# Optimization experiments

Hardware: AMD Instinct MI355X
Metric: run time of the kernel (lower is better)

## Reference

```python
import jax, jax.numpy as jnp
import numpy as np

H = 64   # hidden_dim
E = 5    # num_edge_features
F = 6    # num_node_features
B, W, N = 8, 12, 200
LN_EPS = 1e-5


def _lstm_layer(x, Wih, Whh, bih, bhh):
    # x: [BN, W, Fin] -> full output sequence [BN, W, H] (PyTorch gate order i,f,g,o)
    BN = x.shape[0]
    h0 = jnp.zeros((BN, Whh.shape[1]), x.dtype)
    def step(carry, xt):
        h, c = carry
        g = xt @ Wih.T + h @ Whh.T + (bih + bhh)
        i, f, gg, o = jnp.split(g, 4, axis=-1)
        c = jax.nn.sigmoid(f) * c + jax.nn.sigmoid(i) * jnp.tanh(gg)
        h = jax.nn.sigmoid(o) * jnp.tanh(c)
        return (h, c), h
    _, ys = jax.lax.scan(step, (h0, h0), jnp.swapaxes(x, 0, 1))
    return jnp.swapaxes(ys, 0, 1)


def _layernorm(x, g, b):
    mu = jnp.mean(x, axis=-1, keepdims=True)
    var = jnp.mean(jnp.square(x - mu), axis=-1, keepdims=True)
    return (x - mu) * jax.lax.rsqrt(var + LN_EPS) * g + b


def setup_inputs() -> dict:
    key = jax.random.key(0)
    ks = jax.random.split(key, 32)
    s = 0.05
    d = {
        'node_features': jax.random.normal(ks[0], (B, W, N, F), jnp.float32),
        'edge_features': jax.random.normal(ks[1], (B, W, N, N, E), jnp.float32),
        'adjacency': jax.random.uniform(ks[2], (B, N, N), jnp.float32),
        # LSTM layer 0 (input F) and layer 1 (input H)
        'Wih0': jax.random.normal(ks[3], (4 * H, F), jnp.float32) * s,
        'Whh0': jax.random.normal(ks[4], (4 * H, H), jnp.float32) * s,
        'bih0': jax.random.normal(ks[5], (4 * H,), jnp.float32) * s,
        'bhh0': jax.random.normal(ks[6], (4 * H,), jnp.float32) * s,
        'Wih1': jax.random.normal(ks[7], (4 * H, H), jnp.float32) * s,
        'Whh1': jax.random.normal(ks[8], (4 * H, H), jnp.float32) * s,
        'bih1': jax.random.normal(ks[9], (4 * H,), jnp.float32) * s,
        'bhh1': jax.random.normal(ks[10], (4 * H,), jnp.float32) * s,
        # 2 GCN layers: linear, edge projection, layernorm
        'gcn_W': jax.random.normal(ks[11], (2, H, H), jnp.float32) * s,
        'gcn_b': jax.random.normal(ks[12], (2, H), jnp.float32) * s,
        'ep_W': jax.random.normal(ks[13], (2, H, E), jnp.float32) * s,
        'ep_b': jax.random.normal(ks[14], (2, H), jnp.float32) * s,
        'ln_g': jnp.ones((2, H), jnp.float32),
        'ln_b': jnp.zeros((2, H), jnp.float32),
        # edge MLP: (2H+E) -> H -> H//2 -> 1
        'mlp_W1': jax.random.normal(ks[15], (H, 2 * H + E), jnp.float32) * s,
        'mlp_b1': jax.random.normal(ks[16], (H,), jnp.float32) * s,
        'mlp_W2': jax.random.normal(ks[17], (H // 2, H), jnp.float32) * s,
        'mlp_b2': jax.random.normal(ks[18], (H // 2,), jnp.float32) * s,
        'mlp_W3': jax.random.normal(ks[19], (1, H // 2), jnp.float32) * s,
        'mlp_b3': jax.random.normal(ks[20], (1,), jnp.float32) * s,
    }
    return d


def reference(node_features, edge_features, adjacency,
              Wih0, Whh0, bih0, bhh0, Wih1, Whh1, bih1, bhh1,
              gcn_W, gcn_b, ep_W, ep_b, ln_g, ln_b,
              mlp_W1, mlp_b1, mlp_W2, mlp_b2, mlp_W3, mlp_b3):
    Bn, Wn, Nn, _ = node_features.shape
    # [B,W,N,F] -> [B*N, W, F]
    x = jnp.transpose(node_features, (0, 2, 1, 3)).reshape(Bn * Nn, Wn, -1)
    y0 = _lstm_layer(x, Wih0, Whh0, bih0, bhh0)      # dropout between layers: eval mode (identity)
    y1 = _lstm_layer(y0, Wih1, Whh1, bih1, bhh1)
    h = y1[:, -1, :].reshape(Bn, Nn, H)

    edge_last = edge_features[:, -1]                 # [B,N,N,E]
    for i in range(2):
        edge_h = edge_last @ ep_W[i].T + ep_b[i]     # [B,N,N,H]
        messages = jnp.einsum('bij,bijn->bin', adjacency, edge_h)
        updated = h @ gcn_W[i].T + gcn_b[i] + messages
        h = jax.nn.relu(_layernorm(updated, ln_g[i], ln_b[i]))
        # dropout: eval mode (identity)

    h_i = jnp.broadcast_to(h[:, :, None, :], (Bn, Nn, Nn, H))
    h_j = jnp.broadcast_to(h[:, None, :, :], (Bn, Nn, Nn, H))
    edge_input = jnp.concatenate([h_i, h_j, edge_last], axis=-1)  # [B,N,N,2H+E]
    z = jax.nn.relu(edge_input @ mlp_W1.T + mlp_b1)
    z = jax.nn.relu(z @ mlp_W2.T + mlp_b2)
    logits = (z @ mlp_W3.T + mlp_b3)[..., 0]
    return jax.nn.sigmoid(logits)
```

## Files before the change

### kernel.cpp

```cpp
#include <hip/hip_runtime.h>
#include <math.h>


#define Hd   64
#define Ed   5
#define Fd   6
#define Bd   8
#define Wd   12
#define Nd   200
#define NSEQ (Bd*Nd)
#define NG   (4*Hd)
#define NEDGE (Bd*Nd*Nd)
#define LNEPS 1e-5f

__device__ __forceinline__ float sigm(float x) { return 1.0f / (1.0f + __expf(-x)); }
__device__ __forceinline__ float tanh_fast(float x) {
  float ax = fabsf(x);
  float t  = __expf(-2.0f * ax);
  float r  = (1.0f - t) / (1.0f + t);
  return copysignf(r, x);
}

__global__ __launch_bounds__(256) void k_prep(
    const float* __restrict__ Wih1, const float* __restrict__ gcn_W,
    const float* __restrict__ ep_W, const float* __restrict__ W1,
    float* __restrict__ Wt1, float* __restrict__ gcnWT,
    float* __restrict__ epWT, float* __restrict__ W1aT,
    float* __restrict__ W1bT)
{
  int idx = blockIdx.x * 256 + threadIdx.x;
  if (idx < 16384) {
    int k = idx >> 8, j = idx & 255;
    Wt1[idx] = Wih1[j * Hd + k];
  } else if (idx < 24576) {
    int r0 = idx - 16384;
    int round = r0 >> 12, rem = r0 & 4095;
    int k = rem >> 6, u = rem & 63;
    gcnWT[r0] = gcn_W[round * 4096 + u * 64 + k];
  } else if (idx < 25216) {
    int r0 = idx - 24576;
    int round = r0 / 320, rem = r0 % 320;
    int e = rem >> 6, u = rem & 63;
    epWT[r0] = ep_W[round * 320 + u * Ed + e];
  } else if (idx < 29312) {
    int r0 = idx - 25216;
    int k = r0 >> 6, n = r0 & 63;
    W1aT[r0] = W1[n * 133 + k];
  } else if (idx < 33408) {
    int r0 = idx - 29312;
    int k = r0 >> 6, n = r0 & 63;
    W1bT[r0] = W1[n * 133 + 64 + k];
  }
}

__global__ __launch_bounds__(256, 3) void k_lstm0(
    const float* __restrict__ nf,
    const float* __restrict__ Wih0, const float* __restrict__ Whh0,
    const float* __restrict__ bih0, const float* __restrict__ bhh0,
    float* __restrict__ y0)
{
  __shared__ float x_sh[Wd * Fd];
  __shared__ float h_sh[Hd];
  __shared__ float gate_sh[2][NG];

  const int tid = threadIdx.x;
  const int seq = blockIdx.x;
  const int b = seq / Nd, n = seq % Nd;
  const int u = tid & 63;

  if (tid < Wd * Fd) {
    int t = tid / Fd, f = tid % Fd;
    x_sh[tid] = nf[((b * Wd + t) * Nd + n) * Fd + f];
  }
  h_sh[u] = 0.f;

  const int j = tid;
  float4 wh[16];
  const float4* wrow = (const float4*)(Whh0 + j * Hd);
  #pragma unroll
  for (int q = 0; q < 16; ++q) wh[q] = wrow[q];
  float wx[Fd];
  #pragma unroll
  for (int f = 0; f < Fd; ++f) wx[f] = Wih0[j * Fd + f];
  const float bias = bih0[j] + bhh0[j];
  const int jt = j >> 6;

  float c = 0.f;
  float yreg[Wd];
  __syncthreads();

  for (int t = 0; t < Wd; ++t) {
    const float* xp = x_sh + t * Fd;
    float a0 = bias, a1 = 0.f, a2 = 0.f, a3 = 0.f;
    #pragma unroll
    for (int f = 0; f < Fd; ++f) a1 += xp[f] * wx[f];
    const float4* h4 = (const float4*)h_sh;
    #pragma unroll
    for (int q = 0; q < 16; ++q) {
      float4 hv = h4[q];
      float d = hv.x * wh[q].x + hv.y * wh[q].y + hv.z * wh[q].z + hv.w * wh[q].w;
      if ((q & 3) == 0) a0 += d; else if ((q & 3) == 1) a1 += d;
      else if ((q & 3) == 2) a2 += d; else a3 += d;
    }
    float acc = (a0 + a1) + (a2 + a3);
    gate_sh[t & 1][j] = (jt == 2) ? tanh_fast(acc) : sigm(acc);
    __syncthreads();
    const float* gb = gate_sh[t & 1];
    float iv = gb[u];
    float fv = gb[64 + u];
    float gv = gb[128 + u];
    float ov = gb[192 + u];
    c = fv * c + iv * gv;
    float h = ov * tanh_fast(c);
    h_sh[u] = h;
    yreg[t] = h;
  }
  if (tid < Hd) {
    #pragma unroll
    for (int t = 0; t < Wd; ++t)
      y0[seq * (Wd * Hd) + t * Hd + u] = yreg[t];
  }
}

__global__ __launch_bounds__(256) void k_xproj1(
    const float* __restrict__ y0,
    const float* __restrict__ Wt1,
    const float* __restrict__ bih1, const float* __restrict__ bhh1,
    float* __restrict__ G1)
{
  __shared__ float ysh[64 * 65];
  __shared__ float osh[2 * 64 * 65];

  const int tid  = threadIdx.x;
  const int row0 = blockIdx.x * 64;
  for (int idx = tid; idx < 64 * 64; idx += 256) {
    int r = idx >> 6, k = idx & 63;
    ysh[r * 65 + k] = y0[(row0 + r) * Hd + k];
  }
  __syncthreads();

  const int w = __builtin_amdgcn_readfirstlane(tid >> 6);
  const int r = tid & 63;
  float acc[64];
  #pragma unroll
  for (int c = 0; c < 64; ++c) acc[c] = 0.f;

  const float* wbase = Wt1 + (w << 6);
  #pragma unroll 2
  for (int k = 0; k < 64; ++k) {
    float yv = ysh[r * 65 + k];
    const float* wk = wbase + k * NG;
    #pragma unroll
    for (int c = 0; c < 64; ++c) acc[c] = fmaf(yv, wk[c], acc[c]);
  }
  #pragma unroll
  for (int c = 0; c < 64; ++c) acc[c] += bih1[(w << 6) + c] + bhh1[(w << 6) + c];

  #pragma unroll
  for (int p = 0; p < 2; ++p) {
    __syncthreads();
    if ((w >> 1) == p) {
      float* orow = osh + ((w & 1) * 64 + r) * 65;
      #pragma unroll
      for (int c = 0; c < 64; ++c) orow[c] = acc[c];
    }
    __syncthreads();
    for (int idx = tid; idx < 2 * 64 * 64; idx += 256) {
      int c  = idx & 127;
      int rr = idx >> 7;
      G1[(row0 + rr) * NG + p * 128 + c] =
          osh[((c >> 6) * 64 + rr) * 65 + (c & 63)];
    }
  }
}

__global__ __launch_bounds__(256, 3) void k_lstm1(
    const float* __restrict__ G1,
    const float* __restrict__ Whh1,
    float* __restrict__ hout)
{
  __shared__ float h_sh[Hd];
  __shared__ float gate_sh[2][NG];

  const int tid = threadIdx.x;
  const int seq = blockIdx.x;
  const int u = tid & 63;
  h_sh[u] = 0.f;

  const int j = tid;
  float4 wh[16];
  const float4* wrow = (const float4*)(Whh1 + j * Hd);
  #pragma unroll
  for (int q = 0; q < 16; ++q) wh[q] = wrow[q];
  const int jt = j >> 6;
  float c = 0.f;
  float hlast = 0.f;

  float g_cur = G1[(seq * Wd + 0) * NG + j];
  __syncthreads();

  for (int t = 0; t < Wd; ++t) {
    float g_next = (t + 1 < Wd) ? G1[(seq * Wd + t + 1) * NG + j] : 0.f;
    float a0 = g_cur;
    float a1 = 0.f, a2 = 0.f, a3 = 0.f;
    const float4* h4 = (const float4*)h_sh;
    #pragma unroll
    for (int q = 0; q < 16; ++q) {
      float4 hv = h4[q];
      float d = hv.x * wh[q].x + hv.y * wh[q].y + hv.z * wh[q].z + hv.w * wh[q].w;
      if ((q & 3) == 0) a0 += d; else if ((q & 3) == 1) a1 += d;
      else if ((q & 3) == 2) a2 += d; else a3 += d;
    }
    float acc = (a0 + a1) + (a2 + a3);
    gate_sh[t & 1][j] = (jt == 2) ? tanh_fast(acc) : sigm(acc);
    __syncthreads();
    const float* gb = gate_sh[t & 1];
    float iv = gb[u];
    float fv = gb[64 + u];
    float gv = gb[128 + u];
    float ov = gb[192 + u];
    c = fv * c + iv * gv;
    float h = ov * tanh_fast(c);
    h_sh[u] = h;
    hlast = h;
    g_cur = g_next;
  }
  if (tid < Hd) hout[seq * Hd + u] = hlast;
}

__global__ __launch_bounds__(256) void k_node(
    const float* __restrict__ ef,    const float* __restrict__ adj,
    const float* __restrict__ h0,
    const float* __restrict__ gcnWT, const float* __restrict__ gcn_b,
    const float* __restrict__ epWT,  const float* __restrict__ ep_b,
    const float* __restrict__ ln_g,  const float* __restrict__ ln_b,
    const float* __restrict__ W1aT,  const float* __restrict__ W1bT,
    const float* __restrict__ b1,
    float* __restrict__ uu, float* __restrict__ vt)
{
  __shared__ float ef_sh[Nd * Ed];
  __shared__ float adj_sh[Nd];
  __shared__ float red[4][6];
  __shared__ float w6[6];
  __shared__ float hcur[Hd];

  const int row = blockIdx.x;
  const int b = row / Nd, i = row % Nd;
  const int tid = threadIdx.x;

  const float* efrow = ef + (size_t)(((b * Wd + (Wd - 1)) * Nd + i)) * (Nd * Ed);
  for (int idx = tid; idx < Nd * Ed; idx += 256) ef_sh[idx] = efrow[idx];
  const float* adjrow = adj + (b * Nd + i) * Nd;
  if (tid < Nd) adj_sh[tid] = adjrow[tid];
  if (tid < Hd) hcur[tid] = h0[row * Hd + tid];
  __syncthreads();

  float p[6] = {0.f, 0.f, 0.f, 0.f, 0.f, 0.f};
  if (tid < Nd) {
    float a = adj_sh[tid];
    p[5] = a;
    #pragma unroll
    for (int k = 0; k < Ed; ++k) p[k] = a * ef_sh[tid * Ed + k];
  }
  #pragma unroll
  for (int k = 0; k < 6; ++k) {
    float v = p[k];
    for (int off = 32; off > 0; off >>= 1) v += __shfl_down(v, off);
    p[k] = v;
  }
  if ((tid & 63) == 0) {
    #pragma unroll
    for (int k = 0; k < 6; ++k) red[tid >> 6][k] = p[k];
  }
  __syncthreads();
  if (tid < 6)
    w6[tid] = red[0][tid] + red[1][tid] + red[2][tid] + red[3][tid];
  __syncthreads();

  const int u = tid & 63;
  #pragma unroll
  for (int round = 0; round < 2; ++round) {
    float hnew = 0.f;
    if (tid < 64) {
      const float* gwT = gcnWT + round * 4096;
      const float* ewT = epWT  + round * 320;
      float acc = gcn_b[round * Hd + u] + w6[5] * ep_b[round * Hd + u];
      #pragma unroll
      for (int e = 0; e < Ed; ++e) acc += w6[e] * ewT[e * 64 + u];
      #pragma unroll 8
      for (int k = 0; k < Hd; ++k) acc += hcur[k] * gwT[k * 64 + u];

      float mu = acc;
      #pragma unroll
      for (int off = 1; off < 64; off <<= 1) mu += __shfl_xor(mu, off);
      mu *= (1.f / 64.f);
      float d = acc - mu;
      float var = d * d;
      #pragma unroll
      for (int off = 1; off < 64; off <<= 1) var += __shfl_xor(var, off);
      var *= (1.f / 64.f);
      float v = d * rsqrtf(var + LNEPS) * ln_g[round * Hd + u] + ln_b[round * Hd + u];
      hnew = fmaxf(v, 0.f);
    }
    __syncthreads();
    if (tid < 64) hcur[tid] = hnew;
    __syncthreads();
  }

  if (tid < 64) {
    float acc = b1[tid];
    #pragma unroll 8
    for (int k = 0; k < Hd; ++k) acc += hcur[k] * W1aT[k * 64 + tid];
    uu[row * Hd + tid] = acc;
  } else if (tid < 128) {
    const int n = tid - 64;
    float acc = 0.f;
    #pragma unroll 8
    for (int k = 0; k < Hd; ++k) acc += hcur[k] * W1bT[k * 64 + n];
    vt[n * NSEQ + row] = acc;
  }
}

__global__ __launch_bounds__(256) void k_mlp(
    const float* __restrict__ ef,
    const float* __restrict__ u, const float* __restrict__ vt,
    const float* __restrict__ W1,
    const float* __restrict__ W2, const float* __restrict__ b2,
    const float* __restrict__ W3, const float* __restrict__ b3,
    float* __restrict__ out)
{
  const int idx = blockIdx.x * 256 + threadIdx.x;
  const int b   = idx / (Nd * Nd);
  const int rem = idx - b * Nd * Nd;
  const int i   = rem / Nd;
  const int jj  = rem - i * Nd;

  const float* e = ef + (((b * Wd + (Wd - 1)) * Nd + i) * Nd + jj) * Ed;
  float e5[Ed];
  #pragma unroll
  for (int q = 0; q < Ed; ++q) e5[q] = e[q];

  const float* ur = u + (b * Nd + i) * Hd;
  const int vcol = b * Nd + jj;

  float z1[64];
  #pragma unroll
  for (int k = 0; k < 64; ++k) {
    float acc = ur[k] + vt[k * NSEQ + vcol];
    const float* w1c = W1 + k * 133 + 128;
    #pragma unroll
    for (int q = 0; q < Ed; ++q) acc += e5[q] * w1c[q];
    z1[k] = fmaxf(acc, 0.f);
  }

  float logit = b3[0];
  #pragma unroll 4
  for (int o = 0; o < 32; ++o) {
    float a0 = b2[o], a1 = 0.f, a2 = 0.f, a3 = 0.f;
    const float* w2 = W2 + o * 64;
    #pragma unroll
    for (int k = 0; k < 64; k += 4) {
      a0 += w2[k]     * z1[k];
      a1 += w2[k + 1] * z1[k + 1];
      a2 += w2[k + 2] * z1[k + 2];
      a3 += w2[k + 3] * z1[k + 3];
    }
    float z2 = fmaxf((a0 + a1) + (a2 + a3), 0.f);
    logit += W3[o] * z2;
  }
  out[idx] = 1.f / (1.f + __expf(-logit));
}

extern "C" void kernel_launch(void* const* d_in, const int* in_sizes, int n_in,
                              void* d_out, int out_size, void* d_ws, size_t ws_size,
                              hipStream_t stream) {
  (void)in_sizes; (void)n_in; (void)out_size; (void)ws_size;
  const float* nf   = (const float*)d_in[0];
  const float* ef   = (const float*)d_in[1];
  const float* adj  = (const float*)d_in[2];
  const float* Wih0 = (const float*)d_in[3];
  const float* Whh0 = (const float*)d_in[4];
  const float* bih0 = (const float*)d_in[5];
  const float* bhh0 = (const float*)d_in[6];
  const float* Wih1 = (const float*)d_in[7];
  const float* Whh1 = (const float*)d_in[8];
  const float* bih1 = (const float*)d_in[9];
  const float* bhh1 = (const float*)d_in[10];
  const float* gcnW = (const float*)d_in[11];
  const float* gcnB = (const float*)d_in[12];
  const float* epW  = (const float*)d_in[13];
  const float* epB  = (const float*)d_in[14];
  const float* lnG  = (const float*)d_in[15];
  const float* lnB  = (const float*)d_in[16];
  const float* W1   = (const float*)d_in[17];
  const float* b1   = (const float*)d_in[18];
  const float* W2   = (const float*)d_in[19];
  const float* b2   = (const float*)d_in[20];
  const float* W3   = (const float*)d_in[21];
  const float* b3   = (const float*)d_in[22];
  float* out = (float*)d_out;

  float* ws   = (float*)d_ws;
  float* y0   = ws;
  float* G1   = y0   + 1228800;
  float* Wt1  = G1   + 4915200;
  float* h0   = Wt1  + 16384;
  float* uu   = h0   + 102400;
  float* vt   = uu   + 102400;
  float* gWT  = vt   + 102400;
  float* eWT  = gWT  + 8192;
  float* W1aT = eWT  + 640;
  float* W1bT = W1aT + 4096;

  k_prep  <<<131,  256, 0, stream>>>(Wih1, gcnW, epW, W1,
                                     Wt1, gWT, eWT, W1aT, W1bT);
  k_lstm0 <<<NSEQ, 256, 0, stream>>>(nf, Wih0, Whh0, bih0, bhh0, y0);
  k_xproj1<<<300,  256, 0, stream>>>(y0, Wt1, bih1, bhh1, G1);
  k_lstm1 <<<NSEQ, 256, 0, stream>>>(G1, Whh1, h0);
  k_node  <<<1600, 256, 0, stream>>>(ef, adj, h0, gWT, gcnB, eWT, epB,
                                     lnG, lnB, W1aT, W1bT, b1, uu, vt);
  k_mlp   <<<1250, 256, 0, stream>>>(ef, uu, vt, W1, W2, b2, W3, b3, out);
}
```

Measured before the change: 267.8 us.

## Fuse both LSTM layers into one wavefront-pipelined kernel with 8 sequences per block

Replaces the separate layer-0 LSTM, layer-1 input projection and layer-1 LSTM kernels with a single kernel. Threads 0-255 run layer 0 and threads 256-511 run layer 1 one step behind, with layer 1 computing its input projection on the fly from layer 0's hidden state in shared memory. Each block handles 8 sequences so weights held in registers are reused across them. This removes the y0 and G1 global round-trips and two launches, at the cost of more register pressure from the second weight set and serial per-sequence loops inside each timestep.

```diff
diff --git a/kernel.cpp b/kernel.cpp
--- a/kernel.cpp
+++ b/kernel.cpp
@@ -10,7 +10,7 @@
 #define Nd   200
 #define NSEQ (Bd*Nd)
 #define NG   (4*Hd)
-#define NEDGE (Bd*Nd*Nd)
+#define SEQPB 8
 #define LNEPS 1e-5f
 
 __device__ __forceinline__ float sigm(float x) { return 1.0f / (1.0f + __expf(-x)); }
@@ -22,210 +22,176 @@
 }
 
 __global__ __launch_bounds__(256) void k_prep(
-    const float* __restrict__ Wih1, const float* __restrict__ gcn_W,
-    const float* __restrict__ ep_W, const float* __restrict__ W1,
-    float* __restrict__ Wt1, float* __restrict__ gcnWT,
-    float* __restrict__ epWT, float* __restrict__ W1aT,
-    float* __restrict__ W1bT)
+    const float* __restrict__ gcn_W, const float* __restrict__ ep_W,
+    const float* __restrict__ W1,
+    float* __restrict__ gcnWT, float* __restrict__ epWT,
+    float* __restrict__ W1aT, float* __restrict__ W1bT)
 {
   int idx = blockIdx.x * 256 + threadIdx.x;
-  if (idx < 16384) {
-    int k = idx >> 8, j = idx & 255;
-    Wt1[idx] = Wih1[j * Hd + k];
-  } else if (idx < 24576) {
-    int r0 = idx - 16384;
-    int round = r0 >> 12, rem = r0 & 4095;
+  if (idx < 8192) {
+    int round = idx >> 12, rem = idx & 4095;
     int k = rem >> 6, u = rem & 63;
-    gcnWT[r0] = gcn_W[round * 4096 + u * 64 + k];
-  } else if (idx < 25216) {
-    int r0 = idx - 24576;
+    gcnWT[idx] = gcn_W[round * 4096 + u * 64 + k];
+  } else if (idx < 8832) {
+    int r0 = idx - 8192;
     int round = r0 / 320, rem = r0 % 320;
     int e = rem >> 6, u = rem & 63;
     epWT[r0] = ep_W[round * 320 + u * Ed + e];
-  } else if (idx < 29312) {
-    int r0 = idx - 25216;
+  } else if (idx < 12928) {
+    int r0 = idx - 8832;
     int k = r0 >> 6, n = r0 & 63;
     W1aT[r0] = W1[n * 133 + k];
-  } else if (idx < 33408) {
-    int r0 = idx - 29312;
+  } else if (idx < 17024) {
+    int r0 = idx - 12928;
     int k = r0 >> 6, n = r0 & 63;
     W1bT[r0] = W1[n * 133 + 64 + k];
   }
 }
 
-__global__ __launch_bounds__(256, 3) void k_lstm0(
+__global__ __launch_bounds__(512, 2) void k_lstm_fused(
     const float* __restrict__ nf,
     const float* __restrict__ Wih0, const float* __restrict__ Whh0,
     const float* __restrict__ bih0, const float* __restrict__ bhh0,
-    float* __restrict__ y0)
+    const float* __restrict__ Wih1, const float* __restrict__ Whh1,
+    const float* __restrict__ bih1, const float* __restrict__ bhh1,
+    float* __restrict__ hout)
 {
-  __shared__ float x_sh[Wd * Fd];
-  __shared__ float h_sh[Hd];
-  __shared__ float gate_sh[2][NG];
-
-  const int tid = threadIdx.x;
-  const int seq = blockIdx.x;
-  const int b = seq / Nd, n = seq % Nd;
-  const int u = tid & 63;
-
-  if (tid < Wd * Fd) {
-    int t = tid / Fd, f = tid % Fd;
-    x_sh[tid] = nf[((b * Wd + t) * Nd + n) * Fd + f];
-  }
-  h_sh[u] = 0.f;
-
-  const int j = tid;
+  __shared__ float x_sh[SEQPB][Wd * Fd];
+  __shared__ float h0_sh[SEQPB][Hd];
+  __shared__ float h1_sh[SEQPB][Hd];
+  __shared__ float g0_sh[SEQPB][NG];
+  __shared__ float g1_sh[SEQPB][NG];
+
+  const int tid  = threadIdx.x;
+  const int seq0 = blockIdx.x * SEQPB;
+  const int b    = seq0 / Nd;
+  const int n0   = seq0 % Nd;
+
+  for (int idx = tid; idx < SEQPB * Wd * Fd; idx += 512) {
+    int s = idx / (Wd * Fd), r = idx - s * (Wd * Fd);
+    int t = r / Fd, f = r - t * Fd;
+    x_sh[s][r] = nf[((b * Wd + t) * Nd + (n0 + s)) * Fd + f];
+  }
+  ((float*)h0_sh)[tid >= 512 ? 0 : tid] = 0.f;
+  ((float*)h1_sh)[tid >= 512 ? 0 : tid] = 0.f;
+
+  const bool isL0 = (tid < 256);
+  const int j  = tid & 255;
+  const int jt = j >> 6;
+  const int u  = tid & 63;
+  const int w  = (tid >> 6) & 3;
+
   float4 wh[16];
-  const float4* wrow = (const float4*)(Whh0 + j * Hd);
-  #pragma unroll
-  for (int q = 0; q < 16; ++q) wh[q] = wrow[q];
-  float wx[Fd];
-  #pragma unroll
-  for (int f = 0; f < Fd; ++f) wx[f] = Wih0[j * Fd + f];
-  const float bias = bih0[j] + bhh0[j];
-  const int jt = j >> 6;
-
-  float c = 0.f;
-  float yreg[Wd];
+  float4 wi1[16];
+  float  wx[Fd];
+  float  bias;
+  if (isL0) {
+    const float4* wr = (const float4*)(Whh0 + j * Hd);
+    #pragma unroll
+    for (int q = 0; q < 16; ++q) wh[q] = wr[q];
+    #pragma unroll
+    for (int f = 0; f < Fd; ++f) wx[f] = Wih0[j * Fd + f];
+    bias = bih0[j] + bhh0[j];
+  } else {
+    const float4* wr = (const float4*)(Whh1 + j * Hd);
+    #pragma unroll
+    for (int q = 0; q < 16; ++q) wh[q] = wr[q];
+    const float4* xr = (const float4*)(Wih1 + j * Hd);
+    #pragma unroll
+    for (int q = 0; q < 16; ++q) wi1[q] = xr[q];
+    bias = bih1[j] + bhh1[j];
+  }
+
+  float cA = 0.f, cB = 0.f;
+  float hA = 0.f, hB = 0.f;
   __syncthreads();
 
-  for (int t = 0; t < Wd; ++t) {
-    const float* xp = x_sh + t * Fd;
-    float a0 = bias, a1 = 0.f, a2 = 0.f, a3 = 0.f;
-    #pragma unroll
-    for (int f = 0; f < Fd; ++f) a1 += xp[f] * wx[f];
-    const float4* h4 = (const float4*)h_sh;
-    #pragma unroll
-    for (int q = 0; q < 16; ++q) {
-      float4 hv = h4[q];
-      float d = hv.x * wh[q].x + hv.y * wh[q].y + hv.z * wh[q].z + hv.w * wh[q].w;
-      if ((q & 3) == 0) a0 += d; else if ((q & 3) == 1) a1 += d;
-      else if ((q & 3) == 2) a2 += d; else a3 += d;
-    }
-    float acc = (a0 + a1) + (a2 + a3);
-    gate_sh[t & 1][j] = (jt == 2) ? tanh_fast(acc) : sigm(acc);
-    __syncthreads();
-    const float* gb = gate_sh[t & 1];
-    float iv = gb[u];
-    float fv = gb[64 + u];
-    float gv = gb[128 + u];
-    float ov = gb[192 + u];
-    c = fv * c + iv * gv;
-    float h = ov * tanh_fast(c);
-    h_sh[u] = h;
-    yreg[t] = h;
-  }
-  if (tid < Hd) {
-    #pragma unroll
-    for (int t = 0; t < Wd; ++t)
-      y0[seq * (Wd * Hd) + t * Hd + u] = yreg[t];
-  }
-}
-
-__global__ __launch_bounds__(256) void k_xproj1(
-    const float* __restrict__ y0,
-    const float* __restrict__ Wt1,
-    const float* __restrict__ bih1, const float* __restrict__ bhh1,
-    float* __restrict__ G1)
-{
-  __shared__ float ysh[64 * 65];
-  __shared__ float osh[2 * 64 * 65];
-
-  const int tid  = threadIdx.x;
-  const int row0 = blockIdx.x * 64;
-  for (int idx = tid; idx < 64 * 64; idx += 256) {
-    int r = idx >> 6, k = idx & 63;
-    ysh[r * 65 + k] = y0[(row0 + r) * Hd + k];
-  }
-  __syncthreads();
-
-  const int w = __builtin_amdgcn_readfirstlane(tid >> 6);
-  const int r = tid & 63;
-  float acc[64];
-  #pragma unroll
-  for (int c = 0; c < 64; ++c) acc[c] = 0.f;
-
-  const float* wbase = Wt1 + (w << 6);
-  #pragma unroll 2
-  for (int k = 0; k < 64; ++k) {
-    float yv = ysh[r * 65 + k];
-    const float* wk = wbase + k * NG;
-    #pragma unroll
-    for (int c = 0; c < 64; ++c) acc[c] = fmaf(yv, wk[c], acc[c]);
-  }
-  #pragma unroll
-  for (int c = 0; c < 64; ++c) acc[c] += bih1[(w << 6) + c] + bhh1[(w << 6) + c];
-
-  #pragma unroll
-  for (int p = 0; p < 2; ++p) {
-    __syncthreads();
-    if ((w >> 1) == p) {
-      float* orow = osh + ((w & 1) * 64 + r) * 65;
-      #pragma unroll
-      for (int c = 0; c < 64; ++c) orow[c] = acc[c];
+  for (int t = 0; t <= Wd; ++t) {
+    if (isL0) {
+      if (t < Wd) {
+        #pragma unroll 2
+        for (int s = 0; s < SEQPB; ++s) {
+          const float* xp = &x_sh[s][t * Fd];
+          float a0 = bias, a1 = 0.f, a2 = 0.f, a3 = 0.f;
+          #pragma unroll
+          for (int f = 0; f < Fd; ++f) a1 += xp[f] * wx[f];
+          const float4* h4 = (const float4*)h0_sh[s];
+          #pragma unroll
+          for (int q = 0; q < 16; ++q) {
+            float4 hv = h4[q];
+            float d = hv.x * wh[q].x + hv.y * wh[q].y + hv.z * wh[q].z + hv.w * wh[q].w;
+            if ((q & 3) == 0) a0 += d; else if ((q & 3) == 1) a1 += d;
+            else if ((q & 3) == 2) a2 += d; else a3 += d;
+          }
+          float acc = (a0 + a1) + (a2 + a3);
+          g0_sh[s][j] = (jt == 2) ? tanh_fast(acc) : sigm(acc);
+        }
+      }
+    } else {
+      if (t >= 1) {
+        #pragma unroll 2
+        for (int s = 0; s < SEQPB; ++s) {
+          const float4* y4 = (const float4*)h0_sh[s];
+          float xacc = 0.f;
+          #pragma unroll
+          for (int q = 0; q < 16; ++q) {
+            float4 yv = y4[q];
+            xacc = fmaf(yv.x, wi1[q].x, xacc);
+            xacc = fmaf(yv.y, wi1[q].y, xacc);
+            xacc = fmaf(yv.z, wi1[q].z, xacc);
+            xacc = fmaf(yv.w, wi1[q].w, xacc);
+          }
+          xacc += bias;
+          float a0 = xacc, a1 = 0.f, a2 = 0.f, a3 = 0.f;
+          const float4* h4 = (const float4*)h1_sh[s];
+          #pragma unroll
+          for (int q = 0; q < 16; ++q) {
+            float4 hv = h4[q];
+            float d = hv.x * wh[q].x + hv.y * wh[q].y + hv.z * wh[q].z + hv.w * wh[q].w;
+            if ((q & 3) == 0) a0 += d; else if ((q & 3) == 1) a1 += d;
+            else if ((q & 3) == 2) a2 += d; else a3 += d;
+          }
+          float acc = (a0 + a1) + (a2 + a3);
+          g1_sh[s][j] = (jt == 2) ? tanh_fast(acc) : sigm(acc);
+        }
+      }
     }
     __syncthreads();
-    for (int idx = tid; idx < 2 * 64 * 64; idx += 256) {
-      int c  = idx & 127;
-      int rr = idx >> 7;
-      G1[(row0 + rr) * NG + p * 128 + c] =
-          osh[((c >> 6) * 64 + rr) * 65 + (c & 63)];
+
+    if (isL0) {
+      if (t < Wd) {
+        const float* gb = g0_sh[w];
+        float iv = gb[u], fv = gb[64 + u], gv = gb[128 + u], ov = gb[192 + u];
+        cA = fv * cA + iv * gv;
+        hA = ov * tanh_fast(cA);
+        h0_sh[w][u] = hA;
+        const float* gb2 = g0_sh[w + 4];
+        float iv2 = gb2[u], fv2 = gb2[64 + u], gv2 = gb2[128 + u], ov2 = gb2[192 + u];
+        cB = fv2 * cB + iv2 * gv2;
+        hB = ov2 * tanh_fast(cB);
+        h0_sh[w + 4][u] = hB;
+      }
+    } else {
+      if (t >= 1) {
+        const float* gb = g1_sh[w];
+        float iv = gb[u], fv = gb[64 + u], gv = gb[128 + u], ov = gb[192 + u];
+        cA = fv * cA + iv * gv;
+        hA = ov * tanh_fast(cA);
+        h1_sh[w][u] = hA;
+        const float* gb2 = g1_sh[w + 4];
+        float iv2 = gb2[u], fv2 = gb2[64 + u], gv2 = gb2[128 + u], ov2 = gb2[192 + u];
+        cB = fv2 * cB + iv2 * gv2;
+        hB = ov2 * tanh_fast(cB);
+        h1_sh[w + 4][u] = hB;
+      }
     }
-  }
-}
-
-__global__ __launch_bounds__(256, 3) void k_lstm1(
-    const float* __restrict__ G1,
-    const float* __restrict__ Whh1,
-    float* __restrict__ hout)
-{
-  __shared__ float h_sh[Hd];
-  __shared__ float gate_sh[2][NG];
-
-  const int tid = threadIdx.x;
-  const int seq = blockIdx.x;
-  const int u = tid & 63;
-  h_sh[u] = 0.f;
-
-  const int j = tid;
-  float4 wh[16];
-  const float4* wrow = (const float4*)(Whh1 + j * Hd);
-  #pragma unroll
-  for (int q = 0; q < 16; ++q) wh[q] = wrow[q];
-  const int jt = j >> 6;
-  float c = 0.f;
-  float hlast = 0.f;
-
-  float g_cur = G1[(seq * Wd + 0) * NG + j];
-  __syncthreads();
-
-  for (int t = 0; t < Wd; ++t) {
-    float g_next = (t + 1 < Wd) ? G1[(seq * Wd + t + 1) * NG + j] : 0.f;
-    float a0 = g_cur;
-    float a1 = 0.f, a2 = 0.f, a3 = 0.f;
-    const float4* h4 = (const float4*)h_sh;
-    #pragma unroll
-    for (int q = 0; q < 16; ++q) {
-      float4 hv = h4[q];
-      float d = hv.x * wh[q].x + hv.y * wh[q].y + hv.z * wh[q].z + hv.w * wh[q].w;
-      if ((q & 3) == 0) a0 += d; else if ((q & 3) == 1) a1 += d;
-      else if ((q & 3) == 2) a2 += d; else a3 += d;
-    }
-    float acc = (a0 + a1) + (a2 + a3);
-    gate_sh[t & 1][j] = (jt == 2) ? tanh_fast(acc) : sigm(acc);
     __syncthreads();
-    const float* gb = gate_sh[t & 1];
-    float iv = gb[u];
-    float fv = gb[64 + u];
-    float gv = gb[128 + u];
-    float ov = gb[192 + u];
-    c = fv * c + iv * gv;
-    float h = ov * tanh_fast(c);
-    h_sh[u] = h;
-    hlast = h;
-    g_cur = g_next;
-  }
-  if (tid < Hd) hout[seq * Hd + u] = hlast;
+  }
+
+  if (!isL0) {
+    hout[(seq0 + w) * Hd + u]     = hA;
+    hout[(seq0 + w + 4) * Hd + u] = hB;
+  }
 }
 
 __global__ __launch_bounds__(256) void k_node(
@@ -401,10 +367,7 @@
   float* out = (float*)d_out;
 
   float* ws   = (float*)d_ws;
-  float* y0   = ws;
-  float* G1   = y0   + 1228800;
-  float* Wt1  = G1   + 4915200;
-  float* h0   = Wt1  + 16384;
+  float* h0   = ws;
   float* uu   = h0   + 102400;
   float* vt   = uu   + 102400;
   float* gWT  = vt   + 102400;
@@ -412,12 +375,10 @@
   float* W1aT = eWT  + 640;
   float* W1bT = W1aT + 4096;
 
-  k_prep  <<<131,  256, 0, stream>>>(Wih1, gcnW, epW, W1,
-                                     Wt1, gWT, eWT, W1aT, W1bT);
-  k_lstm0 <<<NSEQ, 256, 0, stream>>>(nf, Wih0, Whh0, bih0, bhh0, y0);
-  k_xproj1<<<300,  256, 0, stream>>>(y0, Wt1, bih1, bhh1, G1);
-  k_lstm1 <<<NSEQ, 256, 0, stream>>>(G1, Whh1, h0);
-  k_node  <<<1600, 256, 0, stream>>>(ef, adj, h0, gWT, gcnB, eWT, epB,
-                                     lnG, lnB, W1aT, W1bT, b1, uu, vt);
-  k_mlp   <<<1250, 256, 0, stream>>>(ef, uu, vt, W1, W2, b2, W3, b3, out);
-}
+  k_prep      <<<67,        256, 0, stream>>>(gcnW, epW, W1, gWT, eWT, W1aT, W1bT);
+  k_lstm_fused<<<NSEQ/SEQPB,512, 0, stream>>>(nf, Wih0, Whh0, bih0, bhh0,
+                                              Wih1, Whh1, bih1, bhh1, h0);
+  k_node      <<<1600,      256, 0, stream>>>(ef, adj, h0, gWT, gcnB, eWT, epB,
+                                              lnG, lnB, W1aT, W1bT, b1, uu, vt);
+  k_mlp       <<<1250,      256, 0, stream>>>(ef, uu, vt, W1, W2, b2, W3, b3, out);
+}
```

Result: no change. 266.0 us (-0.7%).
